# Kernel optimization log

Hardware: AMD Instinct MI355X
Metric: run time of the kernel (lower is better)

Reference implementation:

```python
import jax, jax.numpy as jnp
import numpy as np

N, F, K, FP = 4096, 256, 8, 64  # nodes, in-feat, heads, out-feat per head
NEG_SLOPE = 0.2
MASK_FILL = -1e30  # stand-in for -inf (numerically safe under softmax/vjp)


def setup_inputs() -> dict:
    key = jax.random.key(0)
    k1, k2, k3, k4, k5 = jax.random.split(key, 5)
    x = jax.random.normal(k1, (N, F), dtype=jnp.float32)
    mask = jax.random.randint(k2, (1, N, N), 0, 2).astype(bool)
    idx = jnp.arange(N)
    mask = mask.at[0, idx, idx].set(True)  # self-loops guarantee no empty softmax rows
    W_w = jax.random.normal(k3, (K * FP, F), dtype=jnp.float32) * (1.0 / np.sqrt(F))
    W_b = jnp.zeros((K * FP,), dtype=jnp.float32)
    a_left = jax.random.normal(k4, (1, K, FP), dtype=jnp.float32) * 0.1
    a_right = jax.random.normal(k5, (1, K, FP), dtype=jnp.float32) * 0.1
    return {"x": x, "W_w": W_w, "W_b": W_b, "a_left": a_left, "a_right": a_right, "mask": mask}


def reference(x, W_w, W_b, a_left, a_right, mask):
    k, fp = a_left.shape[1], a_left.shape[2]
    # W(x): (N, K*F') -> (N, K, F')   [dropout p=0.0 -> identity]
    xe = (x @ W_w.T + W_b).reshape(-1, k, fp)
    # additive scores: h_left (K,N,1) + h_right (K,1,N) -> e (K,N,N)
    hl = jnp.einsum('nkf,kf->kn', xe, a_left[0])
    hr = jnp.einsum('nkf,kf->kn', xe, a_right[0])
    e = hl[:, :, None] + hr[:, None, :]
    e = jnp.where(e > 0, e, NEG_SLOPE * e)          # LeakyReLU(0.2)
    e = jnp.where(mask, e, MASK_FILL)               # masked_fill(~mask, -inf)
    a = jax.nn.softmax(e, axis=-1)                  # (K,N,N)
    # weighted sum of neighbor features: (K,N,N) x (N,K,F') -> (N,K,F')
    h_prime = jnp.einsum('knm,mkf->nkf', a, xe)
    h_prime = jax.nn.elu(h_prime)
    # non-final layer: elu again (as in source) then concat heads
    out = jax.nn.elu(h_prime).reshape(-1, k * fp)   # (N, K*F')
    return (out, mask)
```

## Files before the change

### kernel.cpp

```cpp
#include <hip/hip_runtime.h>
#include <hip/hip_bf16.h>

#define N_NODES 4096
#define F_IN    256
#define KH      8
#define KF      512
#define NEG_SLOPE 0.2f

typedef __attribute__((ext_vector_type(8))) short short8;
typedef __attribute__((ext_vector_type(4))) float floatx4;

union S8U4 { short8 v; unsigned u[4]; };

__device__ __forceinline__ unsigned short f2bf(float f) {
    __hip_bfloat16 h = __float2bfloat16(f);
    unsigned short u; __builtin_memcpy(&u, &h, 2);
    return u;
}
__device__ __forceinline__ unsigned packbf2(float w0, float w1) {
    float2 f2; f2.x = w0; f2.y = w1;
    __hip_bfloat162 h2 = __float22bfloat162_rn(f2);
    unsigned u; __builtin_memcpy(&u, &h2, 4);
    return u;
}
__device__ __forceinline__ float asf(unsigned u) {
    float f; __builtin_memcpy(&f, &u, 4);
    return f;
}

__global__ __launch_bounds__(256) void mask_fused(
    const int* __restrict__ mask, float* __restrict__ outm,
    unsigned long long* __restrict__ bits) {
  const size_t base = (size_t)blockIdx.x * 1024;
  const int tid = threadIdx.x;
  #pragma unroll
  for (int c = 0; c < 4; ++c) {
    const size_t e = base + c * 256 + tid;
    const int v = mask[e];
    outm[e] = v ? 1.f : 0.f;
    const unsigned long long b = __ballot(v != 0);
    if ((tid & 63) == 0) {
      const size_t w = e >> 6;
      bits[(w & 63) * (size_t)N_NODES + (w >> 6)] = b;
    }
  }
}

__global__ __launch_bounds__(256) void mask_pack(
    const int* __restrict__ mask, unsigned long long* __restrict__ bits) {
  const size_t idx = (size_t)blockIdx.x * 256 + threadIdx.x;
  const unsigned long long b = __ballot(mask[idx] != 0);
  if ((threadIdx.x & 63) == 0) {
    const size_t w = idx >> 6;
    bits[(w & 63) * (size_t)N_NODES + (w >> 6)] = b;
  }
}
__global__ __launch_bounds__(256) void mask_copy(
    const int* __restrict__ mask, float* __restrict__ outm) {
  const size_t i4 = (size_t)blockIdx.x * 256 + threadIdx.x;
  const int4 mv = ((const int4*)mask)[i4];
  float4 o;
  o.x = mv.x ? 1.f : 0.f; o.y = mv.y ? 1.f : 0.f;
  o.z = mv.z ? 1.f : 0.f; o.w = mv.w ? 1.f : 0.f;
  ((float4*)outm)[i4] = o;
}

__global__ __launch_bounds__(256) void xe_gemm(
    const float* __restrict__ x,
    const float* __restrict__ Ww,
    const float* __restrict__ Wb,
    const float* __restrict__ al,
    const float* __restrict__ ar,
    unsigned short* __restrict__ xeB,
    float* __restrict__ hl,
    unsigned* __restrict__ E12,
    float* __restrict__ bmax) {
  __shared__ float As[32][65];
  __shared__ float Bs[32][65];
  __shared__ float redmax[4];
  const int tid = threadIdx.x;
  const int n0 = blockIdx.x * 64;
  const int j0 = blockIdx.y * 64;
  const int lr = tid >> 2;
  const int lc = (tid & 3) * 8;
  const int ty = tid >> 4;
  const int tx = tid & 15;
  float c[4][4];
  #pragma unroll
  for (int i = 0; i < 4; ++i)
    #pragma unroll
    for (int j = 0; j < 4; ++j) c[i][j] = 0.f;

  for (int f0 = 0; f0 < F_IN; f0 += 32) {
    const float* ap = x  + (size_t)(n0 + lr) * F_IN + f0 + lc;
    const float* bp = Ww + (size_t)(j0 + lr) * F_IN + f0 + lc;
    const float4 a0 = *(const float4*)ap;
    const float4 a1 = *(const float4*)(ap + 4);
    const float4 b0 = *(const float4*)bp;
    const float4 b1 = *(const float4*)(bp + 4);
    __syncthreads();
    As[lc + 0][lr] = a0.x; As[lc + 1][lr] = a0.y;
    As[lc + 2][lr] = a0.z; As[lc + 3][lr] = a0.w;
    As[lc + 4][lr] = a1.x; As[lc + 5][lr] = a1.y;
    As[lc + 6][lr] = a1.z; As[lc + 7][lr] = a1.w;
    Bs[lc + 0][lr] = b0.x; Bs[lc + 1][lr] = b0.y;
    Bs[lc + 2][lr] = b0.z; Bs[lc + 3][lr] = b0.w;
    Bs[lc + 4][lr] = b1.x; Bs[lc + 5][lr] = b1.y;
    Bs[lc + 6][lr] = b1.z; Bs[lc + 7][lr] = b1.w;
    __syncthreads();
    #pragma unroll
    for (int kk = 0; kk < 32; ++kk) {
      const float4 av = *(const float4*)&As[kk][ty * 4];
      const float4 bv = *(const float4*)&Bs[kk][tx * 4];
      const float a4[4] = {av.x, av.y, av.z, av.w};
      const float b4[4] = {bv.x, bv.y, bv.z, bv.w};
      #pragma unroll
      for (int i = 0; i < 4; ++i)
        #pragma unroll
        for (int j = 0; j < 4; ++j) c[i][j] = fmaf(a4[i], b4[j], c[i][j]);
    }
  }
  const float4 wb4 = *(const float4*)(Wb + j0 + tx * 4);
  const float4 al4 = *(const float4*)(al + j0 + tx * 4);
  const float4 ar4 = *(const float4*)(ar + j0 + tx * 4);
  const float wb[4] = {wb4.x, wb4.y, wb4.z, wb4.w};
  const float alv[4] = {al4.x, al4.y, al4.z, al4.w};
  const float arv[4] = {ar4.x, ar4.y, ar4.z, ar4.w};
  float v[4][4];
  float pl[4], pr[4];
  #pragma unroll
  for (int i = 0; i < 4; ++i) {
    float sl = 0.f, sr = 0.f;
    #pragma unroll
    for (int j = 0; j < 4; ++j) {
      v[i][j] = c[i][j] + wb[j];
      sl = fmaf(v[i][j], alv[j], sl);
      sr = fmaf(v[i][j], arv[j], sr);
    }
    pl[i] = sl; pr[i] = sr;
  }
  {
    const int k   = blockIdx.y;
    const int ft  = tx >> 2;
    const int fb  = (tx & 3) * 4;
    const int cc  = blockIdx.x;
    const int h_  = ty >> 3;
    const int qd  = (ty >> 1) & 3;
    const int jj0 = (ty & 1) * 4;
    unsigned short* tile = xeB + ((((size_t)(k * 4 + ft)) * 64 + cc) << 10)
                         + h_ * 512 + qd * 8 + jj0;
    #pragma unroll
    for (int j = 0; j < 4; ++j) {
      ushort4 pk;
      pk.x = f2bf(v[0][j]); pk.y = f2bf(v[1][j]);
      pk.z = f2bf(v[2][j]); pk.w = f2bf(v[3][j]);
      *(ushort4*)(tile + (fb + j) * 32) = pk;
    }
  }
  #pragma unroll
  for (int off = 8; off > 0; off >>= 1) {
    #pragma unroll
    for (int i = 0; i < 4; ++i) {
      pl[i] += __shfl_down(pl[i], off);
      pr[i] += __shfl_down(pr[i], off);
    }
  }
  if (tx == 0) {
    const int k = blockIdx.y;
    float4 o0 = {pl[0], pl[1], pl[2], pl[3]};
    *(float4*)(hl + k * N_NODES + n0 + ty * 4) = o0;
    uint4 ev;
    ev.x = (unsigned)f2bf(__expf(pr[0])) | ((unsigned)f2bf(__expf(NEG_SLOPE * pr[0])) << 16);
    ev.y = (unsigned)f2bf(__expf(pr[1])) | ((unsigned)f2bf(__expf(NEG_SLOPE * pr[1])) << 16);
    ev.z = (unsigned)f2bf(__expf(pr[2])) | ((unsigned)f2bf(__expf(NEG_SLOPE * pr[2])) << 16);
    ev.w = (unsigned)f2bf(__expf(pr[3])) | ((unsigned)f2bf(__expf(NEG_SLOPE * pr[3])) << 16);
    *(uint4*)(E12 + k * N_NODES + n0 + ty * 4) = ev;
  }
  float bm = (tx == 0)
      ? fmaxf(fmaxf(pr[0], pr[1]), fmaxf(pr[2], pr[3])) : -1e30f;
  bm = fmaxf(bm, __shfl_xor(bm, 16));
  bm = fmaxf(bm, __shfl_xor(bm, 32));
  if ((tid & 63) == 0) redmax[tid >> 6] = bm;
  __syncthreads();
  if (tid == 0) {
    bmax[blockIdx.y * 64 + blockIdx.x] =
        fmaxf(fmaxf(redmax[0], redmax[1]), fmaxf(redmax[2], redmax[3]));
  }
}

__global__ __launch_bounds__(256, 4) void gat_attn(
    const unsigned long long* __restrict__ mbitsT,
    const float* __restrict__ hl,
    const float* __restrict__ bmax,
    const unsigned* __restrict__ E12,
    const unsigned short* __restrict__ xeB,
    float* __restrict__ out) {
  __shared__ float lds_acc[4][64][20];
  const int t = threadIdx.x;
  const int w4 = t >> 6;
  const int lane = t & 63;
  const int k  = blockIdx.x >> 8;
  const int rg = blockIdx.x & 255;
  const int n0 = rg * 16;
  const int row = lane & 15;
  const int quad = lane >> 4;
  const int q8 = quad * 8;

  float hm = bmax[k * 64 + lane];
  #pragma unroll
  for (int o = 1; o < 64; o <<= 1) hm = fmaxf(hm, __shfl_xor(hm, o));

  const float hlv = hl[k * N_NODES + n0 + row];
  const float sM = hlv + hm;
  const float Mv = fmaxf(sM, NEG_SLOPE * sM);
  const float c1 = __expf(hlv - Mv);
  const float c2 = __expf(NEG_SLOPE * hlv - Mv);

  const unsigned* E12_k = E12 + k * N_NODES;
  const unsigned long long* mrowT = mbitsT + n0 + row;
  const unsigned short* xeB_k = xeB + (((size_t)k * 4) << 16);

  short8 ones;
  #pragma unroll
  for (int i = 0; i < 8; ++i) ones[i] = (short)0x3F80;

  floatx4 acc[4];
  #pragma unroll
  for (int ft = 0; ft < 4; ++ft) acc[ft] = (floatx4){0.f, 0.f, 0.f, 0.f};
  floatx4 accdp = (floatx4){0.f, 0.f, 0.f, 0.f};

  const int c0 = w4 * 16;
  const int cEnd = c0 + 16;

  uint4 pA, pB, pC, pD;
  unsigned long long pM;
  {
    const unsigned* pe = E12_k + c0 * 64 + q8;
    pA = *(const uint4*)pe;       pB = *(const uint4*)(pe + 4);
    pC = *(const uint4*)(pe + 32); pD = *(const uint4*)(pe + 36);
    pM = mrowT[(size_t)c0 * N_NODES];
  }

  for (int cc = c0; cc < cEnd; ++cc) {
    short8 b0, b1, b2, b3, b4, b5, b6, b7;
    {
      const unsigned short* tb = xeB_k + (((size_t)cc) << 10) + row * 32 + q8;
      b0 = *(const short8*)tb;              b1 = *(const short8*)(tb + 512);
      b2 = *(const short8*)(tb + (64 << 10));      b3 = *(const short8*)(tb + (64 << 10) + 512);
      b4 = *(const short8*)(tb + (128 << 10));     b5 = *(const short8*)(tb + (128 << 10) + 512);
      b6 = *(const short8*)(tb + (192 << 10));     b7 = *(const short8*)(tb + (192 << 10) + 512);
    }
    const uint4 eL0 = pA, eL1 = pB, eH0 = pC, eH1 = pD;
    const unsigned long long mb = pM;
    if (cc + 1 < cEnd) {
      const unsigned* pe = E12_k + (cc + 1) * 64 + q8;
      pA = *(const uint4*)pe;       pB = *(const uint4*)(pe + 4);
      pC = *(const uint4*)(pe + 32); pD = *(const uint4*)(pe + 36);
      pM = mrowT[(size_t)(cc + 1) * N_NODES];
    }
    const unsigned mlo = (unsigned)(mb >> q8);
    const unsigned mhi = (unsigned)(mb >> (32 + q8));
    S8U4 a0, a1;
    {
      const unsigned e[8] = {eL0.x, eL0.y, eL0.z, eL0.w, eL1.x, eL1.y, eL1.z, eL1.w};
      #pragma unroll
      for (int p = 0; p < 4; ++p) {
        const unsigned u0 = e[2 * p], u1 = e[2 * p + 1];
        float w0 = fmaxf(c1 * asf(u0 << 16), c2 * asf(u0 & 0xFFFF0000u));
        float w1 = fmaxf(c1 * asf(u1 << 16), c2 * asf(u1 & 0xFFFF0000u));
        w0 = ((mlo >> (2 * p)) & 1u)     ? w0 : 0.f;
        w1 = ((mlo >> (2 * p + 1)) & 1u) ? w1 : 0.f;
        a0.u[p] = packbf2(w0, w1);
      }
    }
    {
      const unsigned e[8] = {eH0.x, eH0.y, eH0.z, eH0.w, eH1.x, eH1.y, eH1.z, eH1.w};
      #pragma unroll
      for (int p = 0; p < 4; ++p) {
        const unsigned u0 = e[2 * p], u1 = e[2 * p + 1];
        float w0 = fmaxf(c1 * asf(u0 << 16), c2 * asf(u0 & 0xFFFF0000u));
        float w1 = fmaxf(c1 * asf(u1 << 16), c2 * asf(u1 & 0xFFFF0000u));
        w0 = ((mhi >> (2 * p)) & 1u)     ? w0 : 0.f;
        w1 = ((mhi >> (2 * p + 1)) & 1u) ? w1 : 0.f;
        a1.u[p] = packbf2(w0, w1);
      }
    }
    accdp = __builtin_amdgcn_mfma_f32_16x16x32_bf16(a0.v, ones, accdp, 0, 0, 0);
    accdp = __builtin_amdgcn_mfma_f32_16x16x32_bf16(a1.v, ones, accdp, 0, 0, 0);
    acc[0] = __builtin_amdgcn_mfma_f32_16x16x32_bf16(a0.v, b0, acc[0], 0, 0, 0);
    acc[0] = __builtin_amdgcn_mfma_f32_16x16x32_bf16(a1.v, b1, acc[0], 0, 0, 0);
    acc[1] = __builtin_amdgcn_mfma_f32_16x16x32_bf16(a0.v, b2, acc[1], 0, 0, 0);
    acc[1] = __builtin_amdgcn_mfma_f32_16x16x32_bf16(a1.v, b3, acc[1], 0, 0, 0);
    acc[2] = __builtin_amdgcn_mfma_f32_16x16x32_bf16(a0.v, b4, acc[2], 0, 0, 0);
    acc[2] = __builtin_amdgcn_mfma_f32_16x16x32_bf16(a1.v, b5, acc[2], 0, 0, 0);
    acc[3] = __builtin_amdgcn_mfma_f32_16x16x32_bf16(a0.v, b6, acc[3], 0, 0, 0);
    acc[3] = __builtin_amdgcn_mfma_f32_16x16x32_bf16(a1.v, b7, acc[3], 0, 0, 0);
  }

  #pragma unroll
  for (int i = 0; i < 16; ++i) lds_acc[w4][lane][i] = acc[i >> 2][i & 3];
  #pragma unroll
  for (int i = 0; i < 4; ++i) lds_acc[w4][lane][16 + i] = accdp[i];
  __syncthreads();

  #pragma unroll
  for (int j = 0; j < 4; ++j) {
    const int sl = 4 * w4 + j;
    const int row_o = quad * 4 + j;
    float fa = 0.f, dpt = 0.f;
    #pragma unroll
    for (int w2 = 0; w2 < 4; ++w2) {
      fa  += lds_acc[w2][lane][sl];
      dpt += lds_acc[w2][lane][16 + j];
    }
    float v = fa / dpt;
    v = (v > 0.f) ? v : (__expf(v) - 1.f);
    v = (v > 0.f) ? v : (__expf(v) - 1.f);
    out[(size_t)(n0 + row_o) * KF + k * 64 + w4 * 16 + row] = v;
  }
}

extern "C" void kernel_launch(void* const* d_in, const int* in_sizes, int n_in,
                              void* d_out, int out_size, void* d_ws, size_t ws_size,
                              hipStream_t stream) {
  const float* x    = (const float*)d_in[0];
  const float* Ww   = (const float*)d_in[1];
  const float* Wb   = (const float*)d_in[2];
  const float* al   = (const float*)d_in[3];
  const float* ar   = (const float*)d_in[4];
  const int*   mask = (const int*)d_in[5];

  float* out      = (float*)d_out;
  float* out_mask = out + (size_t)N_NODES * KF;

  const bool use_ws = (ws_size >= (8u << 20));
  char* scratch = use_ws ? (char*)d_ws : (char*)out_mask;
  unsigned short* xeB  = (unsigned short*)scratch;
  float*          hl   = (float*)(scratch + (4u << 20));
  unsigned*       E12  = (unsigned*)(hl + KH * N_NODES);
  float*          bmax = (float*)(E12 + KH * N_NODES);
  unsigned long long* mbitsT = (unsigned long long*)(scratch + (5u << 20));

  dim3 ga(N_NODES / 64, KF / 64);
  xe_gemm<<<ga, 256, 0, stream>>>(x, Ww, Wb, al, ar, xeB, hl, E12, bmax);

  if (use_ws) {
    mask_fused<<<(N_NODES * (size_t)N_NODES) / 1024, 256, 0, stream>>>(
        mask, out_mask, mbitsT);
    gat_attn<<<256 * KH, 256, 0, stream>>>(mbitsT, hl, bmax, E12, xeB, out);
  } else {
    mask_pack<<<(N_NODES * (size_t)N_NODES) / 256, 256, 0, stream>>>(mask, mbitsT);
    gat_attn<<<256 * KH, 256, 0, stream>>>(mbitsT, hl, bmax, E12, xeB, out);
    mask_copy<<<(N_NODES * (size_t)N_NODES) / (4 * 256), 256, 0, stream>>>(mask, out_mask);
  }
}
```

Before: 244.2 us.

## Switch attention weights and features from bf16 to fp16 with packed half math

Stores xe features and the exp(hr) factors as fp16 instead of bf16, and splits the exp factors into two separate arrays (EA/EB). The inner loop now computes weights with packed half2 multiply/max and applies the mask with a bitwise AND instead of float selects, then feeds fp16 MFMAs. This is meant to cut VALU work per weight (no fp32 unpack/repack). A bias EBIAS keeps the exponentials inside fp16 range, at the cost of narrower dynamic range and possible overflow or underflow risk.

```diff
diff --git a/kernel.cpp b/kernel.cpp
--- a/kernel.cpp
+++ b/kernel.cpp
@@ -6,26 +6,26 @@
 #define KH      8
 #define KF      512
 #define NEG_SLOPE 0.2f
-
-typedef __attribute__((ext_vector_type(8))) short short8;
+#define EBIAS   4.0f
+
+typedef _Float16 half8v __attribute__((ext_vector_type(8)));
+typedef _Float16 half2v __attribute__((ext_vector_type(2)));
 typedef __attribute__((ext_vector_type(4))) float floatx4;
 
-union S8U4 { short8 v; unsigned u[4]; };
-
-__device__ __forceinline__ unsigned short f2bf(float f) {
-    __hip_bfloat16 h = __float2bfloat16(f);
+union H8U4 { half8v v; unsigned u[4]; };
+
+__device__ __forceinline__ unsigned short f2h(float f) {
+    _Float16 h = (_Float16)f;
     unsigned short u; __builtin_memcpy(&u, &h, 2);
     return u;
 }
-__device__ __forceinline__ unsigned packbf2(float w0, float w1) {
-    float2 f2; f2.x = w0; f2.y = w1;
-    __hip_bfloat162 h2 = __float22bfloat162_rn(f2);
-    unsigned u; __builtin_memcpy(&u, &h2, 4);
+__device__ __forceinline__ half2v asH2(unsigned u) {
+    half2v h; __builtin_memcpy(&h, &u, 4);
+    return h;
+}
+__device__ __forceinline__ unsigned asU(half2v h) {
+    unsigned u; __builtin_memcpy(&u, &h, 4);
     return u;
-}
-__device__ __forceinline__ float asf(unsigned u) {
-    float f; __builtin_memcpy(&f, &u, 4);
-    return f;
 }
 
 __global__ __launch_bounds__(256) void mask_fused(
@@ -73,7 +73,8 @@
     const float* __restrict__ ar,
     unsigned short* __restrict__ xeB,
     float* __restrict__ hl,
-    unsigned* __restrict__ E12,
+    unsigned* __restrict__ EA,
+    unsigned* __restrict__ EB,
     float* __restrict__ bmax) {
   __shared__ float As[32][65];
   __shared__ float Bs[32][65];
@@ -152,8 +153,8 @@
     #pragma unroll
     for (int j = 0; j < 4; ++j) {
       ushort4 pk;
-      pk.x = f2bf(v[0][j]); pk.y = f2bf(v[1][j]);
-      pk.z = f2bf(v[2][j]); pk.w = f2bf(v[3][j]);
+      pk.x = f2h(v[0][j]); pk.y = f2h(v[1][j]);
+      pk.z = f2h(v[2][j]); pk.w = f2h(v[3][j]);
       *(ushort4*)(tile + (fb + j) * 32) = pk;
     }
   }
@@ -169,12 +170,19 @@
     const int k = blockIdx.y;
     float4 o0 = {pl[0], pl[1], pl[2], pl[3]};
     *(float4*)(hl + k * N_NODES + n0 + ty * 4) = o0;
-    uint4 ev;
-    ev.x = (unsigned)f2bf(__expf(pr[0])) | ((unsigned)f2bf(__expf(NEG_SLOPE * pr[0])) << 16);
-    ev.y = (unsigned)f2bf(__expf(pr[1])) | ((unsigned)f2bf(__expf(NEG_SLOPE * pr[1])) << 16);
-    ev.z = (unsigned)f2bf(__expf(pr[2])) | ((unsigned)f2bf(__expf(NEG_SLOPE * pr[2])) << 16);
-    ev.w = (unsigned)f2bf(__expf(pr[3])) | ((unsigned)f2bf(__expf(NEG_SLOPE * pr[3])) << 16);
-    *(uint4*)(E12 + k * N_NODES + n0 + ty * 4) = ev;
+    unsigned short e1[4], e2[4];
+    #pragma unroll
+    for (int i = 0; i < 4; ++i) {
+      e1[i] = f2h(__expf(pr[i] - EBIAS));
+      e2[i] = f2h(__expf(NEG_SLOPE * (pr[i] - EBIAS)));
+    }
+    uint2 wa, wbv;
+    wa.x  = (unsigned)e1[0] | ((unsigned)e1[1] << 16);
+    wa.y  = (unsigned)e1[2] | ((unsigned)e1[3] << 16);
+    wbv.x = (unsigned)e2[0] | ((unsigned)e2[1] << 16);
+    wbv.y = (unsigned)e2[2] | ((unsigned)e2[3] << 16);
+    *(uint2*)(EA + k * 2048 + ((n0 + ty * 4) >> 1)) = wa;
+    *(uint2*)(EB + k * 2048 + ((n0 + ty * 4) >> 1)) = wbv;
   }
   float bm = (tx == 0)
       ? fmaxf(fmaxf(pr[0], pr[1]), fmaxf(pr[2], pr[3])) : -1e30f;
@@ -192,7 +200,8 @@
     const unsigned long long* __restrict__ mbitsT,
     const float* __restrict__ hl,
     const float* __restrict__ bmax,
-    const unsigned* __restrict__ E12,
+    const unsigned* __restrict__ EA,
+    const unsigned* __restrict__ EB,
     const unsigned short* __restrict__ xeB,
     float* __restrict__ out) {
   __shared__ float lds_acc[4][64][20];
@@ -213,88 +222,89 @@
   const float hlv = hl[k * N_NODES + n0 + row];
   const float sM = hlv + hm;
   const float Mv = fmaxf(sM, NEG_SLOPE * sM);
-  const float c1 = __expf(hlv - Mv);
-  const float c2 = __expf(NEG_SLOPE * hlv - Mv);
-
-  const unsigned* E12_k = E12 + k * N_NODES;
-  const unsigned long long* mrowT = mbitsT + n0 + row;
-  const unsigned short* xeB_k = xeB + (((size_t)k * 4) << 16);
-
-  short8 ones;
-  #pragma unroll
-  for (int i = 0; i < 8; ++i) ones[i] = (short)0x3F80;
+  const float c1f = __expf(hlv + EBIAS - Mv);
+  const float c2f = __expf(NEG_SLOPE * (hlv + EBIAS) - Mv);
+  const half2v c1h2 = {(_Float16)c1f, (_Float16)c1f};
+  const half2v c2h2 = {(_Float16)c2f, (_Float16)c2f};
+
+  const int c0 = w4 * 16;
+  const int cEnd = c0 + 16;
+
+  const unsigned* pEA = EA + k * 2048 + c0 * 32 + quad * 4;
+  const unsigned* pEB = EB + k * 2048 + c0 * 32 + quad * 4;
+  const unsigned long long* pM = mbitsT + (size_t)c0 * N_NODES + n0 + row;
+  const unsigned short* pB = xeB + (((size_t)k * 4) << 16)
+                           + ((size_t)c0 << 10) + row * 32 + q8;
+
+  half8v ones;
+  #pragma unroll
+  for (int i = 0; i < 8; ++i) ones[i] = (_Float16)1.0f;
 
   floatx4 acc[4];
   #pragma unroll
   for (int ft = 0; ft < 4; ++ft) acc[ft] = (floatx4){0.f, 0.f, 0.f, 0.f};
   floatx4 accdp = (floatx4){0.f, 0.f, 0.f, 0.f};
 
-  const int c0 = w4 * 16;
-  const int cEnd = c0 + 16;
-
-  uint4 pA, pB, pC, pD;
-  unsigned long long pM;
-  {
-    const unsigned* pe = E12_k + c0 * 64 + q8;
-    pA = *(const uint4*)pe;       pB = *(const uint4*)(pe + 4);
-    pC = *(const uint4*)(pe + 32); pD = *(const uint4*)(pe + 36);
-    pM = mrowT[(size_t)c0 * N_NODES];
-  }
+  uint4 pA0 = *(const uint4*)pEA;
+  uint4 pA1 = *(const uint4*)(pEA + 16);
+  uint4 pB0 = *(const uint4*)pEB;
+  uint4 pB1 = *(const uint4*)(pEB + 16);
+  unsigned long long pMv = *pM;
 
   for (int cc = c0; cc < cEnd; ++cc) {
-    short8 b0, b1, b2, b3, b4, b5, b6, b7;
-    {
-      const unsigned short* tb = xeB_k + (((size_t)cc) << 10) + row * 32 + q8;
-      b0 = *(const short8*)tb;              b1 = *(const short8*)(tb + 512);
-      b2 = *(const short8*)(tb + (64 << 10));      b3 = *(const short8*)(tb + (64 << 10) + 512);
-      b4 = *(const short8*)(tb + (128 << 10));     b5 = *(const short8*)(tb + (128 << 10) + 512);
-      b6 = *(const short8*)(tb + (192 << 10));     b7 = *(const short8*)(tb + (192 << 10) + 512);
-    }
-    const uint4 eL0 = pA, eL1 = pB, eH0 = pC, eH1 = pD;
-    const unsigned long long mb = pM;
+    half8v b0, b1, b2, b3, b4, b5, b6, b7;
+    b0 = *(const half8v*)pB;                     b1 = *(const half8v*)(pB + 512);
+    b2 = *(const half8v*)(pB + (64 << 10));      b3 = *(const half8v*)(pB + (64 << 10) + 512);
+    b4 = *(const half8v*)(pB + (128 << 10));     b5 = *(const half8v*)(pB + (128 << 10) + 512);
+    b6 = *(const half8v*)(pB + (192 << 10));     b7 = *(const half8v*)(pB + (192 << 10) + 512);
+    pB += 1024;
+    const uint4 eA0 = pA0, eA1 = pA1, eB0 = pB0, eB1 = pB1;
+    const unsigned long long mb = pMv;
+    pEA += 32; pEB += 32; pM += N_NODES;
     if (cc + 1 < cEnd) {
-      const unsigned* pe = E12_k + (cc + 1) * 64 + q8;
-      pA = *(const uint4*)pe;       pB = *(const uint4*)(pe + 4);
-      pC = *(const uint4*)(pe + 32); pD = *(const uint4*)(pe + 36);
-      pM = mrowT[(size_t)(cc + 1) * N_NODES];
+      pA0 = *(const uint4*)pEA;
+      pA1 = *(const uint4*)(pEA + 16);
+      pB0 = *(const uint4*)pEB;
+      pB1 = *(const uint4*)(pEB + 16);
+      pMv = *pM;
     }
     const unsigned mlo = (unsigned)(mb >> q8);
     const unsigned mhi = (unsigned)(mb >> (32 + q8));
-    S8U4 a0, a1;
+    H8U4 a0, a1;
     {
-      const unsigned e[8] = {eL0.x, eL0.y, eL0.z, eL0.w, eL1.x, eL1.y, eL1.z, eL1.w};
+      const unsigned ea[4] = {eA0.x, eA0.y, eA0.z, eA0.w};
+      const unsigned eb[4] = {eB0.x, eB0.y, eB0.z, eB0.w};
       #pragma unroll
       for (int p = 0; p < 4; ++p) {
-        const unsigned u0 = e[2 * p], u1 = e[2 * p + 1];
-        float w0 = fmaxf(c1 * asf(u0 << 16), c2 * asf(u0 & 0xFFFF0000u));
-        float w1 = fmaxf(c1 * asf(u1 << 16), c2 * asf(u1 & 0xFFFF0000u));
-        w0 = ((mlo >> (2 * p)) & 1u)     ? w0 : 0.f;
-        w1 = ((mlo >> (2 * p + 1)) & 1u) ? w1 : 0.f;
-        a0.u[p] = packbf2(w0, w1);
+        const half2v w2 = __builtin_elementwise_max(c1h2 * asH2(ea[p]),
+                                                    c2h2 * asH2(eb[p]));
+        const unsigned tb = mlo >> (2 * p);
+        const unsigned sel = (((tb & 1u) | ((tb & 2u) << 15)) * 0xFFFFu);
+        a0.u[p] = asU(w2) & sel;
       }
     }
     {
-      const unsigned e[8] = {eH0.x, eH0.y, eH0.z, eH0.w, eH1.x, eH1.y, eH1.z, eH1.w};
+      const unsigned ea[4] = {eA1.x, eA1.y, eA1.z, eA1.w};
+      const unsigned eb[4] = {eB1.x, eB1.y, eB1.z, eB1.w};
       #pragma unroll
       for (int p = 0; p < 4; ++p) {
-        const unsigned u0 = e[2 * p], u1 = e[2 * p + 1];
-        float w0 = fmaxf(c1 * asf(u0 << 16), c2 * asf(u0 & 0xFFFF0000u));
-        float w1 = fmaxf(c1 * asf(u1 << 16), c2 * asf(u1 & 0xFFFF0000u));
-        w0 = ((mhi >> (2 * p)) & 1u)     ? w0 : 0.f;
-        w1 = ((mhi >> (2 * p + 1)) & 1u) ? w1 : 0.f;
-        a1.u[p] = packbf2(w0, w1);
+        const half2v w2 = __builtin_elementwise_max(c1h2 * asH2(ea[p]),
+                                                    c2h2 * asH2(eb[p]));
+        const unsigned tb = mhi >> (2 * p);
+        const unsigned sel = (((tb & 1u) | ((tb & 2u) << 15)) * 0xFFFFu);
+        a1.u[p] = asU(w2) & sel;
       }
     }
-    accdp = __builtin_amdgcn_mfma_f32_16x16x32_bf16(a0.v, ones, accdp, 0, 0, 0);
-    accdp = __builtin_amdgcn_mfma_f32_16x16x32_bf16(a1.v, ones, accdp, 0, 0, 0);
-    acc[0] = __builtin_amdgcn_mfma_f32_16x16x32_bf16(a0.v, b0, acc[0], 0, 0, 0);
-    acc[0] = __builtin_amdgcn_mfma_f32_16x16x32_bf16(a1.v, b1, acc[0], 0, 0, 0);
-    acc[1] = __builtin_amdgcn_mfma_f32_16x16x32_bf16(a0.v, b2, acc[1], 0, 0, 0);
-    acc[1] = __builtin_amdgcn_mfma_f32_16x16x32_bf16(a1.v, b3, acc[1], 0, 0, 0);
-    acc[2] = __builtin_amdgcn_mfma_f32_16x16x32_bf16(a0.v, b4, acc[2], 0, 0, 0);
-    acc[2] = __builtin_amdgcn_mfma_f32_16x16x32_bf16(a1.v, b5, acc[2], 0, 0, 0);
-    acc[3] = __builtin_amdgcn_mfma_f32_16x16x32_bf16(a0.v, b6, acc[3], 0, 0, 0);
-    acc[3] = __builtin_amdgcn_mfma_f32_16x16x32_bf16(a1.v, b7, acc[3], 0, 0, 0);
+    accdp = __builtin_amdgcn_mfma_f32_16x16x32_f16(a0.v, ones, accdp, 0, 0, 0);
+    accdp = __builtin_amdgcn_mfma_f32_16x16x32_f16(a1.v, ones, accdp, 0, 0, 0);
+    acc[0] = __builtin_amdgcn_mfma_f32_16x16x32_f16(a0.v, b0, acc[0], 0, 0, 0);
+    acc[0] = __builtin_amdgcn_mfma_f32_16x16x32_f16(a1.v, b1, acc[0], 0, 0, 0);
+    acc[1] = __builtin_amdgcn_mfma_f32_16x16x32_f16(a0.v, b2, acc[1], 0, 0, 0);
+    acc[1] = __builtin_amdgcn_mfma_f32_16x16x32_f16(a1.v, b3, acc[1], 0, 0, 0);
+    acc[2] = __builtin_amdgcn_mfma_f32_16x16x32_f16(a0.v, b4, acc[2], 0, 0, 0);
+    acc[2] = __builtin_amdgcn_mfma_f32_16x16x32_f16(a1.v, b5, acc[2], 0, 0, 0);
+    acc[3] = __builtin_amdgcn_mfma_f32_16x16x32_f16(a0.v, b6, acc[3], 0, 0, 0);
+    acc[3] = __builtin_amdgcn_mfma_f32_16x16x32_f16(a1.v, b7, acc[3], 0, 0, 0);
   }
 
   #pragma unroll
@@ -337,20 +347,21 @@
   char* scratch = use_ws ? (char*)d_ws : (char*)out_mask;
   unsigned short* xeB  = (unsigned short*)scratch;
   float*          hl   = (float*)(scratch + (4u << 20));
-  unsigned*       E12  = (unsigned*)(hl + KH * N_NODES);
-  float*          bmax = (float*)(E12 + KH * N_NODES);
+  unsigned*       EA   = (unsigned*)(hl + KH * N_NODES);
+  unsigned*       EB   = EA + KH * 2048;
+  float*          bmax = (float*)(EB + KH * 2048);
   unsigned long long* mbitsT = (unsigned long long*)(scratch + (5u << 20));
 
   dim3 ga(N_NODES / 64, KF / 64);
-  xe_gemm<<<ga, 256, 0, stream>>>(x, Ww, Wb, al, ar, xeB, hl, E12, bmax);
+  xe_gemm<<<ga, 256, 0, stream>>>(x, Ww, Wb, al, ar, xeB, hl, EA, EB, bmax);
 
   if (use_ws) {
     mask_fused<<<(N_NODES * (size_t)N_NODES) / 1024, 256, 0, stream>>>(
         mask, out_mask, mbitsT);
-    gat_attn<<<256 * KH, 256, 0, stream>>>(mbitsT, hl, bmax, E12, xeB, out);
+    gat_attn<<<256 * KH, 256, 0, stream>>>(mbitsT, hl, bmax, EA, EB, xeB, out);
   } else {
     mask_pack<<<(N_NODES * (size_t)N_NODES) / 256, 256, 0, stream>>>(mask, mbitsT);
-    gat_attn<<<256 * KH, 256, 0, stream>>>(mbitsT, hl, bmax, E12, xeB, out);
+    gat_attn<<<256 * KH, 256, 0, stream>>>(mbitsT, hl, bmax, EA, EB, xeB, out);
     mask_copy<<<(N_NODES * (size_t)N_NODES) / (4 * 256), 256, 0, stream>>>(mask, out_mask);
   }
 }
```

New measurement: 242.6 us. No clear change (-0.7%).
